# Optimization experiments

Measured on AMD Instinct MI355X. Metric: run time of the kernel, lower is better.

Reference implementation:

```python
import jax, jax.numpy as jnp
import numpy as np

B, N, K, G = 8, 16384, 16, 4
D_OUT = 128
CQ = CV = 64            # cv must equal d_out//2 for the lpe reshape to work
CQG, CVG = CQ // G, CV // G
C_LPE = D_OUT // (2 * G)  # = CVG = 16
BN_EPS = 1e-5


def setup_inputs() -> dict:
    key = jax.random.key(0)
    ks = jax.random.split(key, 8)
    xyz = jax.random.normal(ks[0], (B, N, 3), dtype=jnp.float32)
    query = jax.random.normal(ks[1], (B, CQ, N), dtype=jnp.float32)
    value = jax.random.normal(ks[2], (B, CV, N, 1), dtype=jnp.float32)
    neigh_idx = jax.random.randint(ks[3], (B, N, K), 0, N, dtype=jnp.int64)
    idx_base = (jnp.arange(B, dtype=jnp.int64) * N).reshape(B, 1, 1)
    lpe_W = jax.random.normal(ks[4], (C_LPE, 10), dtype=jnp.float32) * 0.1
    lpe_b = jnp.zeros((C_LPE,), dtype=jnp.float32)
    bn_gamma = jnp.ones((C_LPE,), dtype=jnp.float32)
    bn_beta = jnp.zeros((C_LPE,), dtype=jnp.float32)
    bn_mean = jnp.zeros((C_LPE,), dtype=jnp.float32)
    bn_var = jnp.ones((C_LPE,), dtype=jnp.float32)
    return {"xyz": xyz, "query": query, "value": value,
            "neigh_idx": neigh_idx, "idx_base": idx_base,
            "lpe_W": lpe_W, "lpe_b": lpe_b, "bn_gamma": bn_gamma,
            "bn_beta": bn_beta, "bn_mean": bn_mean, "bn_var": bn_var}


def _gtl_forward(xyz, query, value, neigh_idx, idx_base,
                 lpe_W, lpe_b, bn_gamma, bn_beta, bn_mean, bn_var):
    b, n, _ = xyz.shape
    k = neigh_idx.shape[-1]
    lq = query.reshape(b, G, CQG, n)                       # [b,g,cqg,n]
    lv = value.reshape(b, G, CVG, n)                       # [b,g,cvg,n]
    xyz_g = jnp.broadcast_to(xyz[:, None].transpose(0, 1, 3, 2), (b, G, 3, n))
    # temp channels: key(cqg) | value(cvg) | xyz(3)
    temp = jnp.concatenate([lq, lv, xyz_g], axis=2)        # [b,g,c,n]
    c = temp.shape[2]
    # flat gather honoring idx_base (batch offsets into b*n)
    flat_idx = (neigh_idx + idx_base).reshape(-1)          # [b*n*k]
    pc_flat = temp.transpose(1, 0, 3, 2).reshape(G, b * n, c)
    feat = pc_flat[:, flat_idx, :].reshape(G, b, n, k, c)
    feat = feat.transpose(1, 0, 4, 2, 3)                   # [b,g,c,n,k]
    lk = feat[:, :, :CQG]                                  # [b,g,cqg,n,k]
    lv_n = feat[:, :, CQG:CQG + CVG]                       # [b,g,cvg,n,k]
    f_xyz = feat[:, :, -3:]                                # [b,g,3,n,k]
    # relative positional encoding -> [b,g,n,k,10]
    neighbor_xyz = f_xyz.transpose(0, 1, 3, 4, 2)          # [b,g,n,k,3]
    xyz_tile = jnp.broadcast_to(xyz[:, None, :, None, :], (b, G, n, k, 3))
    relative_xyz = xyz_tile - neighbor_xyz
    relative_dis = jnp.sqrt(jnp.sum(relative_xyz ** 2, axis=-1, keepdims=True))
    relf = jnp.concatenate([relative_dis, relative_xyz, xyz_tile, neighbor_xyz], axis=-1)
    # permute(0,4,2,1,3) then merge (g,k) -> conv input [b,10,n,g*k]
    relf = relf.transpose(0, 4, 2, 1, 3).reshape(b, 10, n, G * k)
    y = jnp.einsum('oc,bcnm->bonm', lpe_W, relf) + lpe_b[None, :, None, None]
    inv_std = bn_gamma / jnp.sqrt(bn_var + BN_EPS)
    y = (y - bn_mean[None, :, None, None]) * inv_std[None, :, None, None] \
        + bn_beta[None, :, None, None]
    y = jax.nn.relu(y)
    f_enc = y.reshape(b, C_LPE, n, G, k).transpose(0, 3, 1, 2, 4)  # [b,g,cvg,n,k]
    # elementwise attention over neighbors
    la = jax.nn.softmax(jnp.sum(lq[..., None] * lk, axis=2), axis=-1)  # [b,g,n,k]
    lv_cat = jnp.concatenate([lv_n, f_enc], axis=2)        # [b,g,2*cvg,n,k]
    out = jnp.sum(la[:, :, None] * lv_cat, axis=-1).reshape(b, -1, n, 1)
    # attention centrality: scatter-add over neighbor indices
    idx_flat = jnp.broadcast_to(neigh_idx[:, None], (b, G, n, k)).reshape(b, G, n * k)
    att_flat = la.reshape(b, G, n * k)
    centrality = jnp.zeros((b, G, n), dtype=la.dtype).at[
        jnp.arange(b)[:, None, None], jnp.arange(G)[None, :, None], idx_flat
    ].add(att_flat)
    return out, f_enc, centrality


def reference(xyz, query, value, neigh_idx, idx_base,
              lpe_W, lpe_b, bn_gamma, bn_beta, bn_mean, bn_var):
    return _gtl_forward(xyz, query, value, neigh_idx, idx_base,
                        lpe_W, lpe_b, bn_gamma, bn_beta, bn_mean, bn_var)
```

## Files before the change

kernel.cpp:

```cpp
#include <hip/hip_runtime.h>

#define B_    8
#define N_    16384
#define K_    16
#define G_    4
#define CQ_   64
#define CV_   64
#define CQG_  16
#define CVG_  16
#define CLPE_ 16
#define NT_   (B_*G_*N_)

__global__ __launch_bounds__(256) void gtl_transpose(
    const float* __restrict__ query,
    const float* __restrict__ value,
    const float* __restrict__ xyz,
    float*  __restrict__ qT,
    float*  __restrict__ vT,
    float4* __restrict__ xyz4)
{
    const int gid = blockIdx.x * 256 + threadIdx.x;
    const int n   = gid & (N_ - 1);
    const int bg  = gid >> 14;
    const int g   = bg & (G_ - 1);
    const int b   = bg >> 2;

    const float* qb = query + (size_t)b*CQ_*N_ + (size_t)g*CQG_*N_ + n;
    const float* vb = value + (size_t)b*CV_*N_ + (size_t)g*CVG_*N_ + n;
    float4* qo = (float4*)(qT + (size_t)gid * 16);
    float4* vo = (float4*)(vT + (size_t)gid * 16);

    #pragma unroll
    for (int q4 = 0; q4 < 4; ++q4) {
        float4 a, c;
        a.x = qb[(size_t)(q4*4+0)*N_]; a.y = qb[(size_t)(q4*4+1)*N_];
        a.z = qb[(size_t)(q4*4+2)*N_]; a.w = qb[(size_t)(q4*4+3)*N_];
        qo[q4] = a;
        c.x = vb[(size_t)(q4*4+0)*N_]; c.y = vb[(size_t)(q4*4+1)*N_];
        c.z = vb[(size_t)(q4*4+2)*N_]; c.w = vb[(size_t)(q4*4+3)*N_];
        vo[q4] = c;
    }

    if (g == 0) {
        const size_t p = (size_t)b*N_ + n;
        xyz4[p] = make_float4(xyz[p*3+0], xyz[p*3+1], xyz[p*3+2], 0.f);
    }
}

__global__ __launch_bounds__(256) void gtl_main(
    const float*  __restrict__ qT,
    const float*  __restrict__ vT,
    const float4* __restrict__ xyz4,
    const int*    __restrict__ nidx,
    const float*  __restrict__ lpeW,
    const float*  __restrict__ lpeB,
    const float*  __restrict__ bnG,
    const float*  __restrict__ bnB,
    const float*  __restrict__ bnM,
    const float*  __restrict__ bnV,
    float* __restrict__ out,
    float* __restrict__ fenc,
    float* __restrict__ cent)
{
    __shared__ float4 sA[CLPE_];
    __shared__ float4 sB[CLPE_];

    const int t = threadIdx.x;
    if (t < CLPE_) {
        const float scale = bnG[t] * rsqrtf(bnV[t] + 1e-5f);
        const float shift = (lpeB[t] - bnM[t]) * scale + bnB[t];
        const float w0 = lpeW[t*10+0];
        const float w1 = lpeW[t*10+1], w2 = lpeW[t*10+2], w3 = lpeW[t*10+3];
        const float w4 = lpeW[t*10+4], w5 = lpeW[t*10+5], w6 = lpeW[t*10+6];
        const float w7 = lpeW[t*10+7], w8 = lpeW[t*10+8], w9 = lpeW[t*10+9];
        sA[t] = make_float4(scale*(w1+w4), scale*(w2+w5), scale*(w3+w6), shift);
        sB[t] = make_float4(scale*(w7-w1), scale*(w8-w2), scale*(w9-w3), scale*w0);
    }
    __syncthreads();

    const int gid = blockIdx.x * 256 + t;
    const int n   = gid & (N_ - 1);
    const int bg  = gid >> 14;
    const int b   = bg >> 2;

    int idx[K_];
    {
        const int4* ip = (const int4*)(nidx + (size_t)(b*N_ + n) * K_);
        #pragma unroll
        for (int q4 = 0; q4 < K_/4; ++q4) {
            const int4 v = ip[q4];
            idx[q4*4+0] = v.x; idx[q4*4+1] = v.y;
            idx[q4*4+2] = v.z; idx[q4*4+3] = v.w;
        }
    }

    const float4* qslab = (const float4*)(qT + (size_t)bg * N_ * 16);
    const float4 lq0 = qslab[(size_t)n*4+0];
    const float4 lq1 = qslab[(size_t)n*4+1];
    const float4 lq2 = qslab[(size_t)n*4+2];
    const float4 lq3 = qslab[(size_t)n*4+3];

    float la[K_];
    #pragma unroll 4
    for (int k = 0; k < K_; ++k) {
        const float4* qj = qslab + (size_t)idx[k]*4;
        const float4 a = qj[0], bq = qj[1], cq = qj[2], dq = qj[3];
        float s;
        s = lq0.x*a.x;            s = fmaf(lq0.y, a.y, s);
        s = fmaf(lq0.z, a.z, s);  s = fmaf(lq0.w, a.w, s);
        s = fmaf(lq1.x, bq.x, s); s = fmaf(lq1.y, bq.y, s);
        s = fmaf(lq1.z, bq.z, s); s = fmaf(lq1.w, bq.w, s);
        s = fmaf(lq2.x, cq.x, s); s = fmaf(lq2.y, cq.y, s);
        s = fmaf(lq2.z, cq.z, s); s = fmaf(lq2.w, cq.w, s);
        s = fmaf(lq3.x, dq.x, s); s = fmaf(lq3.y, dq.y, s);
        s = fmaf(lq3.z, dq.z, s); s = fmaf(lq3.w, dq.w, s);
        la[k] = s;
    }

    float m = la[0];
    #pragma unroll
    for (int k = 1; k < K_; ++k) m = fmaxf(m, la[k]);
    float ssum = 0.f;
    #pragma unroll
    for (int k = 0; k < K_; ++k) { const float e = __expf(la[k] - m); la[k] = e; ssum += e; }
    const float inv = 1.f / ssum;
    #pragma unroll
    for (int k = 0; k < K_; ++k) la[k] *= inv;

    {
        float* cb = cent + (size_t)bg * N_;
        #pragma unroll
        for (int k = 0; k < K_; ++k) atomicAdd(cb + idx[k], la[k]);
    }

    const float4 cpt = xyz4[(size_t)b*N_ + n];
    float basec[CLPE_];
    #pragma unroll
    for (int c = 0; c < CLPE_; ++c) {
        const float4 a = sA[c];
        basec[c] = fmaf(a.x, cpt.x, fmaf(a.y, cpt.y, fmaf(a.z, cpt.z, a.w)));
    }

    const float4* vslab = (const float4*)(vT + (size_t)bg * N_ * 16);
    float4 nbr[K_];
    float accV[CVG_];
    #pragma unroll
    for (int c = 0; c < CVG_; ++c) accV[c] = 0.f;

    #pragma unroll 2
    for (int k = 0; k < K_; ++k) {
        const int j = idx[k];
        const float4 p = xyz4[(size_t)b*N_ + j];
        const float rx = cpt.x - p.x, ry = cpt.y - p.y, rz = cpt.z - p.z;
        const float d  = sqrtf(fmaf(rx,rx, fmaf(ry,ry, rz*rz)));
        nbr[k] = make_float4(p.x, p.y, p.z, d);
        const float w = la[k];
        const float4* vj = vslab + (size_t)j*4;
        const float4 v0 = vj[0], v1 = vj[1], v2 = vj[2], v3 = vj[3];
        accV[0]  = fmaf(w, v0.x, accV[0]);  accV[1]  = fmaf(w, v0.y, accV[1]);
        accV[2]  = fmaf(w, v0.z, accV[2]);  accV[3]  = fmaf(w, v0.w, accV[3]);
        accV[4]  = fmaf(w, v1.x, accV[4]);  accV[5]  = fmaf(w, v1.y, accV[5]);
        accV[6]  = fmaf(w, v1.z, accV[6]);  accV[7]  = fmaf(w, v1.w, accV[7]);
        accV[8]  = fmaf(w, v2.x, accV[8]);  accV[9]  = fmaf(w, v2.y, accV[9]);
        accV[10] = fmaf(w, v2.z, accV[10]); accV[11] = fmaf(w, v2.w, accV[11]);
        accV[12] = fmaf(w, v3.x, accV[12]); accV[13] = fmaf(w, v3.y, accV[13]);
        accV[14] = fmaf(w, v3.z, accV[14]); accV[15] = fmaf(w, v3.w, accV[15]);
    }

    float* fe = fenc + ((size_t)bg * CLPE_ * N_ + n) * K_;
    float* ob = out  + (size_t)bg * (CVG_ + CLPE_) * N_ + n;

    #pragma unroll 2
    for (int c = 0; c < CLPE_; ++c) {
        const float4 wB = sB[c];
        const float base = basec[c];
        float e[K_];
        float acc = 0.f;
        #pragma unroll
        for (int k = 0; k < K_; ++k) {
            const float4 p = nbr[k];
            float tt = base;
            tt = fmaf(wB.x, p.x, tt);
            tt = fmaf(wB.y, p.y, tt);
            tt = fmaf(wB.z, p.z, tt);
            tt = fmaf(wB.w, p.w, tt);
            tt = fmaxf(tt, 0.f);
            e[k] = tt;
            acc  = fmaf(la[k], tt, acc);
        }
        float4* fo = (float4*)(fe + (size_t)c * (N_ * K_));
        fo[0] = make_float4(e[0],  e[1],  e[2],  e[3]);
        fo[1] = make_float4(e[4],  e[5],  e[6],  e[7]);
        fo[2] = make_float4(e[8],  e[9],  e[10], e[11]);
        fo[3] = make_float4(e[12], e[13], e[14], e[15]);
        ob[(size_t)(CVG_ + c) * N_] = acc;
    }

    #pragma unroll
    for (int c = 0; c < CVG_; ++c) ob[(size_t)c * N_] = accV[c];
}

__global__ __launch_bounds__(256) void gtl_fallback(
    const float* __restrict__ xyz,
    const float* __restrict__ query,
    const float* __restrict__ value,
    const int*   __restrict__ nidx,
    const float* __restrict__ lpeW,
    const float* __restrict__ lpeB,
    const float* __restrict__ bnG,
    const float* __restrict__ bnB,
    const float* __restrict__ bnM,
    const float* __restrict__ bnV,
    float* __restrict__ out,
    float* __restrict__ fenc,
    float* __restrict__ cent)
{
    __shared__ float4 sA[CLPE_];
    __shared__ float4 sB[CLPE_];
    const int t = threadIdx.x;
    if (t < CLPE_) {
        const float scale = bnG[t] * rsqrtf(bnV[t] + 1e-5f);
        const float shift = (lpeB[t] - bnM[t]) * scale + bnB[t];
        const float w0 = lpeW[t*10+0];
        const float w1 = lpeW[t*10+1], w2 = lpeW[t*10+2], w3 = lpeW[t*10+3];
        const float w4 = lpeW[t*10+4], w5 = lpeW[t*10+5], w6 = lpeW[t*10+6];
        const float w7 = lpeW[t*10+7], w8 = lpeW[t*10+8], w9 = lpeW[t*10+9];
        sA[t] = make_float4(scale*(w1+w4), scale*(w2+w5), scale*(w3+w6), shift);
        sB[t] = make_float4(scale*(w7-w1), scale*(w8-w2), scale*(w9-w3), scale*w0);
    }
    __syncthreads();
    const int gid = blockIdx.x * 256 + t;
    const int n   = gid & (N_ - 1);
    const int bg  = gid >> 14;
    const int g   = bg & (G_ - 1);
    const int b   = bg >> 2;
    const float cx = xyz[(size_t)(b*N_ + n)*3 + 0];
    const float cy = xyz[(size_t)(b*N_ + n)*3 + 1];
    const float cz = xyz[(size_t)(b*N_ + n)*3 + 2];
    int idx[K_];
    const int4* ip = (const int4*)(nidx + (size_t)(b*N_ + n) * K_);
    #pragma unroll
    for (int q4 = 0; q4 < K_/4; ++q4) {
        const int4 v = ip[q4];
        idx[q4*4+0] = v.x; idx[q4*4+1] = v.y; idx[q4*4+2] = v.z; idx[q4*4+3] = v.w;
    }
    const float* qb = query + (size_t)b*CQ_*N_ + (size_t)g*CQG_*N_;
    float lq[CQG_];
    #pragma unroll
    for (int c = 0; c < CQG_; ++c) lq[c] = qb[(size_t)c*N_ + n];
    float la[K_];
    #pragma unroll 4
    for (int k = 0; k < K_; ++k) {
        const float* qj = qb + idx[k];
        float s = 0.f;
        #pragma unroll
        for (int c = 0; c < CQG_; ++c) s = fmaf(lq[c], qj[(size_t)c*N_], s);
        la[k] = s;
    }
    float m = la[0];
    #pragma unroll
    for (int k = 1; k < K_; ++k) m = fmaxf(m, la[k]);
    float ssum = 0.f;
    #pragma unroll
    for (int k = 0; k < K_; ++k) { const float e = __expf(la[k] - m); la[k] = e; ssum += e; }
    const float inv = 1.f / ssum;
    #pragma unroll
    for (int k = 0; k < K_; ++k) la[k] *= inv;
    float* cb = cent + (size_t)bg * N_;
    #pragma unroll
    for (int k = 0; k < K_; ++k) atomicAdd(cb + idx[k], la[k]);
    float basec[CLPE_];
    #pragma unroll
    for (int c = 0; c < CLPE_; ++c) {
        const float4 a = sA[c];
        basec[c] = fmaf(a.x, cx, fmaf(a.y, cy, fmaf(a.z, cz, a.w)));
    }
    const float* vb = value + (size_t)b*CV_*N_ + (size_t)g*CVG_*N_;
    float accV[CVG_], accE[CLPE_];
    #pragma unroll
    for (int c = 0; c < CLPE_; ++c) { accV[c] = 0.f; accE[c] = 0.f; }
    float* fe = fenc + ((size_t)bg * CLPE_ * N_ + n) * K_;
    #pragma unroll 2
    for (int k = 0; k < K_; ++k) {
        const int j = idx[k];
        const float nx = xyz[(size_t)(b*N_ + j)*3 + 0];
        const float ny = xyz[(size_t)(b*N_ + j)*3 + 1];
        const float nz = xyz[(size_t)(b*N_ + j)*3 + 2];
        const float rx = cx - nx, ry = cy - ny, rz = cz - nz;
        const float d  = sqrtf(rx*rx + ry*ry + rz*rz);
        const float w  = la[k];
        const float* vj = vb + j;
        #pragma unroll
        for (int c = 0; c < CLPE_; ++c) {
            const float4 bb = sB[c];
            float e = basec[c];
            e = fmaf(bb.x, nx, e); e = fmaf(bb.y, ny, e);
            e = fmaf(bb.z, nz, e); e = fmaf(bb.w, d,  e);
            e = fmaxf(e, 0.f);
            fe[(size_t)c*(N_*K_) + k] = e;
            accE[c] = fmaf(w, e, accE[c]);
            accV[c] = fmaf(w, vj[(size_t)c*N_], accV[c]);
        }
    }
    float* ob = out + (size_t)bg * (CVG_ + CLPE_) * N_ + n;
    #pragma unroll
    for (int c = 0; c < CVG_; ++c)  ob[(size_t)c*N_]        = accV[c];
    #pragma unroll
    for (int c = 0; c < CLPE_; ++c) ob[(size_t)(CVG_+c)*N_] = accE[c];
}

extern "C" void kernel_launch(void* const* d_in, const int* in_sizes, int n_in,
                              void* d_out, int out_size, void* d_ws, size_t ws_size,
                              hipStream_t stream) {
    (void)in_sizes; (void)n_in; (void)out_size;

    const float* xyz   = (const float*)d_in[0];
    const float* query = (const float*)d_in[1];
    const float* value = (const float*)d_in[2];
    const int*   nidx  = (const int*)  d_in[3];
    const float* lpeW  = (const float*)d_in[5];
    const float* lpeB  = (const float*)d_in[6];
    const float* bnG   = (const float*)d_in[7];
    const float* bnB   = (const float*)d_in[8];
    const float* bnM   = (const float*)d_in[9];
    const float* bnV   = (const float*)d_in[10];

    float* out  = (float*)d_out;
    float* fenc = out  + (size_t)B_ * (G_*(CVG_+CLPE_)) * N_;
    float* cent = fenc + (size_t)B_ * G_ * CLPE_ * N_ * K_;

    hipMemsetAsync(cent, 0, sizeof(float) * (size_t)B_ * G_ * N_, stream);

    const size_t qT_bytes  = (size_t)NT_ * 16 * sizeof(float);
    const size_t vT_bytes  = qT_bytes;
    const size_t xyz4_bytes = (size_t)B_ * N_ * sizeof(float4);
    const size_t need = qT_bytes + vT_bytes + xyz4_bytes;

    const int grid = NT_ / 256;

    if (ws_size >= need) {
        float*  qT   = (float*)d_ws;
        float*  vT   = qT + (size_t)NT_ * 16;
        float4* xyz4 = (float4*)(vT + (size_t)NT_ * 16);
        hipLaunchKernelGGL(gtl_transpose, dim3(grid), dim3(256), 0, stream,
                           query, value, xyz, qT, vT, xyz4);
        hipLaunchKernelGGL(gtl_main, dim3(grid), dim3(256), 0, stream,
                           qT, vT, xyz4, nidx, lpeW, lpeB, bnG, bnB, bnM, bnV,
                           out, fenc, cent);
    } else {
        hipLaunchKernelGGL(gtl_fallback, dim3(grid), dim3(256), 0, stream,
                           xyz, query, value, nidx, lpeW, lpeB, bnG, bnB, bnM, bnV,
                           out, fenc, cent);
    }
}
```

Measured before the change: 1.220 ms.

## Tile transpose through LDS, fuse centrality zeroing, remap blocks per XCD, use nontemporal stores

The prep kernel now stages 64-point tiles of query and value in shared memory so that both the reads and the float4 writes are coalesced, and it also zeroes the centrality buffer, which removes the separate memset. The main kernel remaps block IDs so that each of the 8 XCDs handles whole (batch, group) slices, aiming to keep gathered neighbor data local to that XCD's L2. The large f_enc and out writes switch to nontemporal stores to reduce cache pollution. The risks are a less even load spread if the XCD mapping assumption does not hold, and the extra LDS use in prep.

```diff
diff --git a/kernel.cpp b/kernel.cpp
--- a/kernel.cpp
+++ b/kernel.cpp
@@ -11,40 +11,67 @@
 #define CLPE_ 16
 #define NT_   (B_*G_*N_)
 
-__global__ __launch_bounds__(256) void gtl_transpose(
+typedef float f4v __attribute__((ext_vector_type(4)));
+
+static __device__ __forceinline__ void nt_store4(float* p, float a, float b,
+                                                 float c, float d) {
+    f4v v = {a, b, c, d};
+    __builtin_nontemporal_store(v, (f4v*)p);
+}
+static __device__ __forceinline__ void nt_store1(float* p, float a) {
+    __builtin_nontemporal_store(a, p);
+}
+
+__global__ __launch_bounds__(256) void gtl_prep(
     const float* __restrict__ query,
     const float* __restrict__ value,
     const float* __restrict__ xyz,
-    float*  __restrict__ qT,
-    float*  __restrict__ vT,
-    float4* __restrict__ xyz4)
+    float4* __restrict__ qT4,
+    float4* __restrict__ vT4,
+    float4* __restrict__ xyz4,
+    float*  __restrict__ cent)
 {
-    const int gid = blockIdx.x * 256 + threadIdx.x;
-    const int n   = gid & (N_ - 1);
-    const int bg  = gid >> 14;
-    const int g   = bg & (G_ - 1);
-    const int b   = bg >> 2;
-
-    const float* qb = query + (size_t)b*CQ_*N_ + (size_t)g*CQG_*N_ + n;
-    const float* vb = value + (size_t)b*CV_*N_ + (size_t)g*CVG_*N_ + n;
-    float4* qo = (float4*)(qT + (size_t)gid * 16);
-    float4* vo = (float4*)(vT + (size_t)gid * 16);
-
-    #pragma unroll
-    for (int q4 = 0; q4 < 4; ++q4) {
-        float4 a, c;
-        a.x = qb[(size_t)(q4*4+0)*N_]; a.y = qb[(size_t)(q4*4+1)*N_];
-        a.z = qb[(size_t)(q4*4+2)*N_]; a.w = qb[(size_t)(q4*4+3)*N_];
-        qo[q4] = a;
-        c.x = vb[(size_t)(q4*4+0)*N_]; c.y = vb[(size_t)(q4*4+1)*N_];
-        c.z = vb[(size_t)(q4*4+2)*N_]; c.w = vb[(size_t)(q4*4+3)*N_];
-        vo[q4] = c;
-    }
-
-    if (g == 0) {
-        const size_t p = (size_t)b*N_ + n;
-        xyz4[p] = make_float4(xyz[p*3+0], xyz[p*3+1], xyz[p*3+2], 0.f);
-    }
+    __shared__ float sq[CQG_][68];
+    __shared__ float sv[CVG_][68];
+
+    const int t    = threadIdx.x;
+    const int bg   = blockIdx.x >> 8;
+    const int tile = blockIdx.x & 255;
+    const int n0   = tile << 6;
+    const int g    = bg & (G_ - 1);
+    const int b    = bg >> 2;
+
+    const int row = t >> 6;
+    const int col = t & 63;
+
+    const float* qb = query + (size_t)b*CQ_*N_ + (size_t)g*CQG_*N_ + n0;
+    const float* vb = value + (size_t)b*CV_*N_ + (size_t)g*CVG_*N_ + n0;
+
+    #pragma unroll
+    for (int cc = 0; cc < 4; ++cc) {
+        const int c = (cc << 2) + row;
+        sq[c][col] = qb[(size_t)c*N_ + col];
+        sv[c][col] = vb[(size_t)c*N_ + col];
+    }
+
+    if (t < 64) {
+        cent[(size_t)bg*N_ + n0 + t] = 0.f;
+        if (g == 0) {
+            const size_t pp = (size_t)b*N_ + n0 + t;
+            xyz4[pp] = make_float4(xyz[pp*3+0], xyz[pp*3+1], xyz[pp*3+2], 0.f);
+        }
+    }
+
+    __syncthreads();
+
+    const int p    = t >> 2;
+    const int quad = t & 3;
+    const int cb   = quad << 2;
+    const float4 oq = make_float4(sq[cb+0][p], sq[cb+1][p], sq[cb+2][p], sq[cb+3][p]);
+    const float4 ov = make_float4(sv[cb+0][p], sv[cb+1][p], sv[cb+2][p], sv[cb+3][p]);
+    const size_t o = ((size_t)bg*N_ + n0 + p)*4 + quad;
+    qT4[o] = oq;
+    vT4[o] = ov;
 }
 
 __global__ __launch_bounds__(256) void gtl_main(
@@ -78,10 +105,12 @@
     }
     __syncthreads();
 
-    const int gid = blockIdx.x * 256 + t;
-    const int n   = gid & (N_ - 1);
-    const int bg  = gid >> 14;
-    const int b   = bg >> 2;
+    const int wid  = blockIdx.x;
+    const int xcd  = wid & 7;
+    const int slot = wid >> 3;
+    const int bg   = (xcd << 2) | (slot >> 6);
+    const int n    = ((slot & 63) << 8) | t;
+    const int b    = bg >> 2;
 
     int idx[K_];
     {
@@ -188,16 +217,16 @@
             e[k] = tt;
             acc  = fmaf(la[k], tt, acc);
         }
-        float4* fo = (float4*)(fe + (size_t)c * (N_ * K_));
-        fo[0] = make_float4(e[0],  e[1],  e[2],  e[3]);
-        fo[1] = make_float4(e[4],  e[5],  e[6],  e[7]);
-        fo[2] = make_float4(e[8],  e[9],  e[10], e[11]);
-        fo[3] = make_float4(e[12], e[13], e[14], e[15]);
-        ob[(size_t)(CVG_ + c) * N_] = acc;
-    }
-
-    #pragma unroll
-    for (int c = 0; c < CVG_; ++c) ob[(size_t)c * N_] = accV[c];
+        float* fo = fe + (size_t)c * (N_ * K_);
+        nt_store4(fo + 0,  e[0],  e[1],  e[2],  e[3]);
+        nt_store4(fo + 4,  e[4],  e[5],  e[6],  e[7]);
+        nt_store4(fo + 8,  e[8],  e[9],  e[10], e[11]);
+        nt_store4(fo + 12, e[12], e[13], e[14], e[15]);
+        nt_store1(ob + (size_t)(CVG_ + c) * N_, acc);
+    }
+
+    #pragma unroll
+    for (int c = 0; c < CVG_; ++c) nt_store1(ob + (size_t)c * N_, accV[c]);
 }
 
 __global__ __launch_bounds__(256) void gtl_fallback(
@@ -329,26 +358,25 @@
     float* fenc = out  + (size_t)B_ * (G_*(CVG_+CLPE_)) * N_;
     float* cent = fenc + (size_t)B_ * G_ * CLPE_ * N_ * K_;
 
-    hipMemsetAsync(cent, 0, sizeof(float) * (size_t)B_ * G_ * N_, stream);
-
-    const size_t qT_bytes  = (size_t)NT_ * 16 * sizeof(float);
-    const size_t vT_bytes  = qT_bytes;
+    const size_t qT_bytes   = (size_t)NT_ * 16 * sizeof(float);
+    const size_t vT_bytes   = qT_bytes;
     const size_t xyz4_bytes = (size_t)B_ * N_ * sizeof(float4);
     const size_t need = qT_bytes + vT_bytes + xyz4_bytes;
-
-    const int grid = NT_ / 256;
 
     if (ws_size >= need) {
         float*  qT   = (float*)d_ws;
         float*  vT   = qT + (size_t)NT_ * 16;
         float4* xyz4 = (float4*)(vT + (size_t)NT_ * 16);
-        hipLaunchKernelGGL(gtl_transpose, dim3(grid), dim3(256), 0, stream,
-                           query, value, xyz, qT, vT, xyz4);
-        hipLaunchKernelGGL(gtl_main, dim3(grid), dim3(256), 0, stream,
+        const int prep_grid = NT_ / 64;
+        const int main_grid = NT_ / 256;
+        hipLaunchKernelGGL(gtl_prep, dim3(prep_grid), dim3(256), 0, stream,
+                           query, value, xyz, (float4*)qT, (float4*)vT, xyz4, cent);
+        hipLaunchKernelGGL(gtl_main, dim3(main_grid), dim3(256), 0, stream,
                            qT, vT, xyz4, nidx, lpeW, lpeB, bnG, bnB, bnM, bnV,
                            out, fenc, cent);
     } else {
-        hipLaunchKernelGGL(gtl_fallback, dim3(grid), dim3(256), 0, stream,
+        hipMemsetAsync(cent, 0, sizeof(float) * (size_t)B_ * G_ * N_, stream);
+        hipLaunchKernelGGL(gtl_fallback, dim3(NT_/256), dim3(256), 0, stream,
                            xyz, query, value, nidx, lpeW, lpeB, bnG, bnB, bnM, bnV,
                            out, fenc, cent);
     }
```

Measured after the change: 1.232 ms. Within noise of the previous version (+1.0%).
